# Optimization experiments

Measured on AMD Instinct MI355X. Metric: run time of the kernel, lower is better.

Reference implementation:

```python
import jax, jax.numpy as jnp
import numpy as np

K = 256
TAU = 1.0


def setup_inputs() -> dict:
    key = jax.random.key(0)
    scores = jax.random.normal(key, (32, 2048), dtype=jnp.float32)
    return {"scores": scores}


def reference(scores) -> jnp.ndarray:
    # scores: [B, dim]
    bsize, dim = scores.shape
    s = scores[:, :, None]  # [B, dim, 1]
    # B_i = sum_j |s_i - s_j|  -> [B, dim, 1]
    A = jnp.abs(s - scores[:, None, :])  # [B, dim, dim]
    Bsum = jnp.sum(A, axis=-1, keepdims=True)  # [B, dim, 1]
    # scaling: (dim + 1 - 2*(i+1)) for i in 0..k-1
    scaling = (dim + 1 - 2 * (jnp.arange(K) + 1)).astype(scores.dtype)  # [k]
    C = s * scaling[None, None, :]  # [B, dim, k] (outer product)
    P_max = jnp.transpose(C - Bsum, (0, 2, 1))  # [B, k, dim]
    P_hat = jax.nn.softmax(P_max / TAU, axis=-1)
    return P_hat
```

## Files before the change

kernel.cpp:

```cpp
#include <hip/hip_runtime.h>
#include <math.h>

#define DIM 2048
#define NB 32
#define NK 256
#define KPB 2

__global__ __launch_bounds__(256) void bsum_kernel(const float* __restrict__ scores,
                                                   float* __restrict__ bsum) {
    __shared__ float4 srow[DIM / 4];
    const int b = blockIdx.y;
    const int t = threadIdx.x;
    const float* row = scores + b * DIM;

    srow[t]       = ((const float4*)row)[t];
    srow[t + 256] = ((const float4*)row)[t + 256];
    __syncthreads();

    const int i = blockIdx.x * 256 + t;
    const float xi = ((const float*)srow)[i];

    float a0 = 0.f, a1 = 0.f, a2 = 0.f, a3 = 0.f;
    #pragma unroll 4
    for (int jj = 0; jj < DIM / 4; ++jj) {
        const float4 xj = srow[jj];
        a0 += fabsf(xi - xj.x);
        a1 += fabsf(xi - xj.y);
        a2 += fabsf(xi - xj.z);
        a3 += fabsf(xi - xj.w);
    }
    bsum[b * DIM + i] = (a0 + a1) + (a2 + a3);
}

__global__ __launch_bounds__(64) void softmax_kernel(const float* __restrict__ scores,
                                                     const float* __restrict__ bsum,
                                                     float* __restrict__ out) {
    const int b  = blockIdx.y;
    const int k0 = blockIdx.x * KPB;
    const int t  = threadIdx.x;

    const float4* s4  = (const float4*)(scores + b * DIM);
    const float4* bs4 = (const float4*)(bsum   + b * DIM);

    float4 sv[8], bv[8];
    #pragma unroll
    for (int q = 0; q < 8; ++q) {
        sv[q] = s4[t + 64 * q];
        bv[q] = bs4[t + 64 * q];
    }

    #pragma unroll
    for (int kk = 0; kk < KPB; ++kk) {
        const int k = k0 + kk;
        const float scale = (float)(DIM - 1 - 2 * k);

        float e[32];
        #pragma unroll
        for (int q = 0; q < 8; ++q) {
            e[4 * q + 0] = fmaf(sv[q].x, scale, -bv[q].x);
            e[4 * q + 1] = fmaf(sv[q].y, scale, -bv[q].y);
            e[4 * q + 2] = fmaf(sv[q].z, scale, -bv[q].z);
            e[4 * q + 3] = fmaf(sv[q].w, scale, -bv[q].w);
        }

        float m0 = e[0], m1 = e[1], m2 = e[2], m3 = e[3];
        #pragma unroll
        for (int j = 4; j < 32; j += 4) {
            m0 = fmaxf(m0, e[j + 0]);
            m1 = fmaxf(m1, e[j + 1]);
            m2 = fmaxf(m2, e[j + 2]);
            m3 = fmaxf(m3, e[j + 3]);
        }
        float m = fmaxf(fmaxf(m0, m1), fmaxf(m2, m3));
        #pragma unroll
        for (int off = 32; off > 0; off >>= 1) m = fmaxf(m, __shfl_xor(m, off, 64));

        float s0 = 0.f, s1 = 0.f, s2 = 0.f, s3 = 0.f;
        #pragma unroll
        for (int j = 0; j < 32; j += 4) {
            e[j + 0] = __expf(e[j + 0] - m); s0 += e[j + 0];
            e[j + 1] = __expf(e[j + 1] - m); s1 += e[j + 1];
            e[j + 2] = __expf(e[j + 2] - m); s2 += e[j + 2];
            e[j + 3] = __expf(e[j + 3] - m); s3 += e[j + 3];
        }
        float s = (s0 + s1) + (s2 + s3);
        #pragma unroll
        for (int off = 32; off > 0; off >>= 1) s += __shfl_xor(s, off, 64);

        const float inv = 1.f / s;
        float4* o4 = (float4*)(out + ((size_t)(b * NK + k)) * DIM);
        #pragma unroll
        for (int q = 0; q < 8; ++q) {
            float4 o;
            o.x = e[4 * q + 0] * inv;
            o.y = e[4 * q + 1] * inv;
            o.z = e[4 * q + 2] * inv;
            o.w = e[4 * q + 3] * inv;
            o4[t + 64 * q] = o;
        }
    }
}

extern "C" void kernel_launch(void* const* d_in, const int* in_sizes, int n_in,
                              void* d_out, int out_size, void* d_ws, size_t ws_size,
                              hipStream_t stream) {
    const float* scores = (const float*)d_in[0];
    float* out  = (float*)d_out;
    float* bsum = (float*)d_ws;

    bsum_kernel<<<dim3(8, NB), 256, 0, stream>>>(scores, bsum);
    softmax_kernel<<<dim3(NK / KPB, NB), 64, 0, stream>>>(scores, bsum, out);
}
```

Baseline: 97.47 us.

## Use nontemporal output stores, one k per wave, and drop LDS staging in bsum

The bsum kernel now reads the row straight from global memory with uniform addresses, which should become scalar or broadcast loads, instead of staging it in LDS first. The softmax kernel changes from 64-thread blocks handling two k values each to 256-thread blocks where each wave handles a single k. Output rows are written with nontemporal stores to avoid polluting the cache with the 64MB output. The trade-off is that each k now reloads the score and bsum rows, and the uniform global loads in bsum may be slower than LDS.

```diff
diff --git a/kernel.cpp b/kernel.cpp
--- a/kernel.cpp
+++ b/kernel.cpp
@@ -4,100 +4,84 @@
 #define DIM 2048
 #define NB 32
 #define NK 256
-#define KPB 2
+
+typedef float vf4 __attribute__((ext_vector_type(4)));
 
 __global__ __launch_bounds__(256) void bsum_kernel(const float* __restrict__ scores,
                                                    float* __restrict__ bsum) {
-    __shared__ float4 srow[DIM / 4];
     const int b = blockIdx.y;
-    const int t = threadIdx.x;
-    const float* row = scores + b * DIM;
-
-    srow[t]       = ((const float4*)row)[t];
-    srow[t + 256] = ((const float4*)row)[t + 256];
-    __syncthreads();
-
-    const int i = blockIdx.x * 256 + t;
-    const float xi = ((const float*)srow)[i];
+    const int i = blockIdx.x * 256 + threadIdx.x;
+    const float* __restrict__ row = scores + b * DIM;
+    const float xi = row[i];
 
     float a0 = 0.f, a1 = 0.f, a2 = 0.f, a3 = 0.f;
-    #pragma unroll 4
-    for (int jj = 0; jj < DIM / 4; ++jj) {
-        const float4 xj = srow[jj];
-        a0 += fabsf(xi - xj.x);
-        a1 += fabsf(xi - xj.y);
-        a2 += fabsf(xi - xj.z);
-        a3 += fabsf(xi - xj.w);
+    #pragma unroll 8
+    for (int j = 0; j < DIM; j += 4) {
+        a0 += fabsf(xi - row[j + 0]);
+        a1 += fabsf(xi - row[j + 1]);
+        a2 += fabsf(xi - row[j + 2]);
+        a3 += fabsf(xi - row[j + 3]);
     }
     bsum[b * DIM + i] = (a0 + a1) + (a2 + a3);
 }
 
-__global__ __launch_bounds__(64) void softmax_kernel(const float* __restrict__ scores,
-                                                     const float* __restrict__ bsum,
-                                                     float* __restrict__ out) {
-    const int b  = blockIdx.y;
-    const int k0 = blockIdx.x * KPB;
-    const int t  = threadIdx.x;
+__global__ __launch_bounds__(256) void softmax_kernel(const float* __restrict__ scores,
+                                                      const float* __restrict__ bsum,
+                                                      float* __restrict__ out) {
+    const int b = blockIdx.y;
+    const int w = threadIdx.x >> 6;
+    const int t = threadIdx.x & 63;
+    const int k = blockIdx.x * 4 + w;
+    const float scale = (float)(DIM - 1 - 2 * k);
 
-    const float4* s4  = (const float4*)(scores + b * DIM);
-    const float4* bs4 = (const float4*)(bsum   + b * DIM);
+    const vf4* __restrict__ s4  = (const vf4*)(scores + b * DIM);
+    const vf4* __restrict__ bs4 = (const vf4*)(bsum   + b * DIM);
 
-    float4 sv[8], bv[8];
+    float e[32];
     #pragma unroll
     for (int q = 0; q < 8; ++q) {
-        sv[q] = s4[t + 64 * q];
-        bv[q] = bs4[t + 64 * q];
+        const vf4 sv = s4[t + 64 * q];
+        const vf4 bv = bs4[t + 64 * q];
+        e[4 * q + 0] = fmaf(sv.x, scale, -bv.x);
+        e[4 * q + 1] = fmaf(sv.y, scale, -bv.y);
+        e[4 * q + 2] = fmaf(sv.z, scale, -bv.z);
+        e[4 * q + 3] = fmaf(sv.w, scale, -bv.w);
     }
 
+    float m0 = e[0], m1 = e[1], m2 = e[2], m3 = e[3];
     #pragma unroll
-    for (int kk = 0; kk < KPB; ++kk) {
-        const int k = k0 + kk;
-        const float scale = (float)(DIM - 1 - 2 * k);
+    for (int j = 4; j < 32; j += 4) {
+        m0 = fmaxf(m0, e[j + 0]);
+        m1 = fmaxf(m1, e[j + 1]);
+        m2 = fmaxf(m2, e[j + 2]);
+        m3 = fmaxf(m3, e[j + 3]);
+    }
+    float m = fmaxf(fmaxf(m0, m1), fmaxf(m2, m3));
+    #pragma unroll
+    for (int off = 32; off > 0; off >>= 1) m = fmaxf(m, __shfl_xor(m, off, 64));
 
-        float e[32];
-        #pragma unroll
-        for (int q = 0; q < 8; ++q) {
-            e[4 * q + 0] = fmaf(sv[q].x, scale, -bv[q].x);
-            e[4 * q + 1] = fmaf(sv[q].y, scale, -bv[q].y);
-            e[4 * q + 2] = fmaf(sv[q].z, scale, -bv[q].z);
-            e[4 * q + 3] = fmaf(sv[q].w, scale, -bv[q].w);
-        }
+    float s0 = 0.f, s1 = 0.f, s2 = 0.f, s3 = 0.f;
+    #pragma unroll
+    for (int j = 0; j < 32; j += 4) {
+        e[j + 0] = __expf(e[j + 0] - m); s0 += e[j + 0];
+        e[j + 1] = __expf(e[j + 1] - m); s1 += e[j + 1];
+        e[j + 2] = __expf(e[j + 2] - m); s2 += e[j + 2];
+        e[j + 3] = __expf(e[j + 3] - m); s3 += e[j + 3];
+    }
+    float s = (s0 + s1) + (s2 + s3);
+    #pragma unroll
+    for (int off = 32; off > 0; off >>= 1) s += __shfl_xor(s, off, 64);
 
-        float m0 = e[0], m1 = e[1], m2 = e[2], m3 = e[3];
-        #pragma unroll
-        for (int j = 4; j < 32; j += 4) {
-            m0 = fmaxf(m0, e[j + 0]);
-            m1 = fmaxf(m1, e[j + 1]);
-            m2 = fmaxf(m2, e[j + 2]);
-            m3 = fmaxf(m3, e[j + 3]);
-        }
-        float m = fmaxf(fmaxf(m0, m1), fmaxf(m2, m3));
-        #pragma unroll
-        for (int off = 32; off > 0; off >>= 1) m = fmaxf(m, __shfl_xor(m, off, 64));
-
-        float s0 = 0.f, s1 = 0.f, s2 = 0.f, s3 = 0.f;
-        #pragma unroll
-        for (int j = 0; j < 32; j += 4) {
-            e[j + 0] = __expf(e[j + 0] - m); s0 += e[j + 0];
-            e[j + 1] = __expf(e[j + 1] - m); s1 += e[j + 1];
-            e[j + 2] = __expf(e[j + 2] - m); s2 += e[j + 2];
-            e[j + 3] = __expf(e[j + 3] - m); s3 += e[j + 3];
-        }
-        float s = (s0 + s1) + (s2 + s3);
-        #pragma unroll
-        for (int off = 32; off > 0; off >>= 1) s += __shfl_xor(s, off, 64);
-
-        const float inv = 1.f / s;
-        float4* o4 = (float4*)(out + ((size_t)(b * NK + k)) * DIM);
-        #pragma unroll
-        for (int q = 0; q < 8; ++q) {
-            float4 o;
-            o.x = e[4 * q + 0] * inv;
-            o.y = e[4 * q + 1] * inv;
-            o.z = e[4 * q + 2] * inv;
-            o.w = e[4 * q + 3] * inv;
-            o4[t + 64 * q] = o;
-        }
+    const float inv = 1.f / s;
+    vf4* o4 = (vf4*)(out + ((size_t)(b * NK + k)) * DIM);
+    #pragma unroll
+    for (int q = 0; q < 8; ++q) {
+        vf4 o;
+        o.x = e[4 * q + 0] * inv;
+        o.y = e[4 * q + 1] * inv;
+        o.z = e[4 * q + 2] * inv;
+        o.w = e[4 * q + 3] * inv;
+        __builtin_nontemporal_store(o, &o4[t + 64 * q]);
     }
 }
 
@@ -109,5 +93,5 @@
     float* bsum = (float*)d_ws;
 
     bsum_kernel<<<dim3(8, NB), 256, 0, stream>>>(scores, bsum);
-    softmax_kernel<<<dim3(NK / KPB, NB), 64, 0, stream>>>(scores, bsum, out);
+    softmax_kernel<<<dim3(NK / 4, NB), 256, 0, stream>>>(scores, bsum, out);
 }
```

New measurement: 107.7 us. +10.5%, slower.
